# Optimization experiments

Measured on AMD Instinct MI355X. Metric: run time of the kernel, lower is better.

The kernel has to match this reference:

```python
import jax, jax.numpy as jnp
import numpy as np

N0, N1, N2, N3 = 600000, 100000, 20000, 4096
E0, E1, E2 = 1500000, 200000, 40960
D_IN, D_H, D_OUT = 100, 256, 47


def setup_inputs() -> dict:
    key = jax.random.key(0)
    ks = jax.random.split(key, 16)
    inp = {
        "x": jax.random.normal(ks[0], (N0, D_IN), jnp.float32),
        "ei0_src": jax.random.randint(ks[1], (E0,), 0, N0, jnp.int32),
        "ei0_dst": jax.random.randint(ks[2], (E0,), 0, N1, jnp.int32),
        "ei1_src": jax.random.randint(ks[3], (E1,), 0, N1, jnp.int32),
        "ei1_dst": jax.random.randint(ks[4], (E1,), 0, N2, jnp.int32),
        "ei2_src": jax.random.randint(ks[5], (E2,), 0, N2, jnp.int32),
        "ei2_dst": jax.random.randint(ks[6], (E2,), 0, N3, jnp.int32),
        "Wl0": jax.random.normal(ks[7], (D_IN, D_H), jnp.float32) * 0.1,
        "Wr0": jax.random.normal(ks[8], (D_IN, D_H), jnp.float32) * 0.1,
        "b0": jnp.zeros((D_H,), jnp.float32),
        "Wl1": jax.random.normal(ks[9], (D_H, D_H), jnp.float32) * 0.06,
        "Wr1": jax.random.normal(ks[10], (D_H, D_H), jnp.float32) * 0.06,
        "b1": jnp.zeros((D_H,), jnp.float32),
        "Wl2": jax.random.normal(ks[11], (D_H, D_OUT), jnp.float32) * 0.06,
        "Wr2": jax.random.normal(ks[12], (D_H, D_OUT), jnp.float32) * 0.06,
        "b2": jnp.zeros((D_OUT,), jnp.float32),
    }
    return inp


def _sage_layer(x_src, x_tgt, src, dst, n_tgt, Wl, Wr, b):
    # PyG SAGEConv (mean aggr): out = lin_l(mean_{j in N(i)} x_j) + lin_r(x_i)
    msgs = x_src[src]                                   # [E, d] gather
    s = jax.ops.segment_sum(msgs, dst, num_segments=n_tgt)
    cnt = jax.ops.segment_sum(jnp.ones((src.shape[0],), x_src.dtype), dst,
                              num_segments=n_tgt)[:, None]
    mean = s / jnp.maximum(cnt, 1.0)
    return mean @ Wl + x_tgt @ Wr + b


def reference(x, ei0_src, ei0_dst, ei1_src, ei1_dst, ei2_src, ei2_dst,
              Wl0, Wr0, b0, Wl1, Wr1, b1, Wl2, Wr2, b2):
    h = _sage_layer(x, x[:N1], ei0_src, ei0_dst, N1, Wl0, Wr0, b0)
    h = jax.nn.relu(h)  # dropout is identity in eval mode
    h = _sage_layer(h, h[:N2], ei1_src, ei1_dst, N2, Wl1, Wr1, b1)
    h = jax.nn.relu(h)
    h = _sage_layer(h, h[:N3], ei2_src, ei2_dst, N3, Wl2, Wr2, b2)
    return jax.nn.log_softmax(h, axis=-1)
```

## Files before the change

kernel.cpp:

```cpp
#include <hip/hip_runtime.h>

#define NN0 600000
#define NN1 100000
#define NN2 20000
#define NN3 4096
#define EE0 1500000
#define EE1 200000
#define EE2 40960
#define DIN 100
#define DH  256
#define DOUT 47
#define NTOT (NN1 + NN2 + NN3)

#define RNG 16384
#define CH0 32768
#define NC0 46
#define R0  7
#define CH1 16384
#define NC1 13
#define R1  2
#define CH2 8192
#define NC2 5
#define R2  1
#define HL0 (NC0 * R0)
#define HL1 (NC1 * R1)
#define HL2 (NC2 * R2)
#define HLT (HL0 + HL1 + HL2)
#define NGMAX 46
#define PACKB 27

#define NB0 98
#define NB1 20
#define NB2 4
#define NBT 122

#define HB0 5860
#define HB1 782
#define HB2 160
#define HBE (HB0 + HB1 + HB2)
#define CONVB 3072

typedef unsigned int uint;
typedef unsigned short ushort;
typedef __attribute__((ext_vector_type(8))) short bhalf8;
typedef __attribute__((ext_vector_type(4))) float f32x4;

union U16B {
    uint2  u2[2];
    uint4  u4;
    bhalf8 s8;
    ushort us[8];
};

__device__ __forceinline__ ushort f2bf(float f) {
    uint u = __float_as_uint(f);
    uint r = (u + 0x7FFFu + ((u >> 16) & 1u)) >> 16;
    return (ushort)r;
}
__device__ __forceinline__ float bf2f(uint bits16) {
    return __uint_as_float(bits16 << 16);
}

__device__ __forceinline__ void pack_one(const float* B, int K, int N, int NB,
                                         ushort* out, int bid, int l) {
    int kstep = bid / NB;
    int c = bid % NB;
    U16B v;
    #pragma unroll
    for (int j = 0; j < 8; ++j) {
        int k = kstep * 32 + ((l >> 4) << 3) + j;
        int col = (c << 4) | (l & 15);
        float f = (k < K && col < N) ? B[(size_t)k * N + col] : 0.0f;
        v.us[j] = f2bf(f);
    }
    *reinterpret_cast<bhalf8*>(out + ((size_t)bid * 64 + l) * 8) = v.s8;
}

__global__ __launch_bounds__(1024)
void hist_pack(const int* __restrict__ e0d, const int* __restrict__ e1d,
               const int* __restrict__ e2d, int* __restrict__ cntp,
               int* __restrict__ pos0, int* __restrict__ pos1,
               int* __restrict__ pos2,
               const float* __restrict__ Wl0, const float* __restrict__ Wr0,
               const float* __restrict__ Wl1, const float* __restrict__ Wr1,
               const float* __restrict__ Wl2, const float* __restrict__ Wr2,
               ushort* Bp0l, ushort* Bp0r, ushort* Bp1l, ushort* Bp1r,
               ushort* Bp2l, ushort* Bp2r) {
    __shared__ int lcnt[RNG];
    int b = blockIdx.x, tid = threadIdx.x;
    if (b >= HLT) {
        int bid = (b - HLT) * 16 + (tid >> 6);
        int l = tid & 63;
        if (bid < 64)       pack_one(Wl0, DIN, DH,  16, Bp0l, bid,       l);
        else if (bid < 128) pack_one(Wr0, DIN, DH,  16, Bp0r, bid - 64,  l);
        else if (bid < 256) pack_one(Wl1, DH,  DH,  16, Bp1l, bid - 128, l);
        else if (bid < 384) pack_one(Wr1, DH,  DH,  16, Bp1r, bid - 256, l);
        else if (bid < 408) pack_one(Wl2, DH,  DOUT, 3, Bp2l, bid - 384, l);
        else if (bid < 432) pack_one(Wr2, DH,  DOUT, 3, Bp2r, bid - 408, l);
        return;
    }
    const int* dstp; int E, CH, c, r, nbase, layerN;
    int* pos;
    if (b < HL0) {
        dstp = e0d; E = EE0; CH = CH0; c = b / R0; r = b % R0;
        nbase = 0; layerN = NN1; pos = pos0;
    } else if (b < HL0 + HL1) {
        int bb = b - HL0;
        dstp = e1d; E = EE1; CH = CH1; c = bb / R1; r = bb % R1;
        nbase = NN1; layerN = NN2; pos = pos1;
    } else {
        int bb = b - HL0 - HL1;
        dstp = e2d; E = EE2; CH = CH2; c = bb; r = 0;
        nbase = NN1 + NN2; layerN = NN3; pos = pos2;
    }
    for (int i = tid; i < RNG; i += 1024) lcnt[i] = 0;
    __syncthreads();
    int rbase = r * RNG;
    long long ebase = (long long)c * CH;
    for (int i = tid; i < CH; i += 1024) {
        int e = (int)(ebase + i);
        if (e < E) {
            int d = dstp[e];
            unsigned li = (unsigned)(d - rbase);
            if (li < RNG) pos[e] = atomicAdd(&lcnt[li], 1);
        }
    }
    __syncthreads();
    for (int i = tid; i < RNG; i += 1024) {
        int node = rbase + i;
        if (node < layerN)
            cntp[(size_t)c * NTOT + nbase + node] = lcnt[i];
    }
}

__device__ __forceinline__ void layer_of(int b, int& lb, int& n, int& po, int& cb) {
    if (b < NB0)      { lb = b;        n = NN1; po = 0;         cb = 0; }
    else if (b < NB0 + NB1) { lb = b - NB0;  n = NN2; po = NB0; cb = NN1; }
    else              { lb = b - NB0 - NB1; n = NN3; po = NB0 + NB1; cb = NN1 + NN2; }
}

__global__ __launch_bounds__(256)
void combScan1(int* __restrict__ cntp, int* __restrict__ cntAll,
               int* __restrict__ part) {
    int lb, n, po, cb;
    layer_of(blockIdx.x, lb, n, po, cb);
    int ng = (cb == 0) ? NC0 : (cb == NN1) ? NC1 : NC2;
    int base = lb * 1024;
    int sum = 0;
    #pragma unroll
    for (int jj = 0; jj < 4; ++jj) {
        int idx = base + threadIdx.x * 4 + jj;
        if (idx < n) {
            int i = cb + idx;
            int run = 0;
            for (int g = 0; g < ng; ++g) {
                size_t id = (size_t)g * NTOT + i;
                int v = cntp[id];
                cntp[id] = run;
                run += v;
            }
            cntAll[i] = run;
            sum += run;
        }
    }
    __shared__ int s[256];
    s[threadIdx.x] = sum;
    __syncthreads();
    for (int off = 128; off; off >>= 1) {
        if (threadIdx.x < off) s[threadIdx.x] += s[threadIdx.x + off];
        __syncthreads();
    }
    if (threadIdx.x == 0) part[po + lb] = s[0];
}

__global__ __launch_bounds__(256)
void scan3L(const int* __restrict__ cntAll, const int* __restrict__ part,
            int* __restrict__ rp0, int* __restrict__ rp1, int* __restrict__ rp2) {
    int lb, n, po, cb;
    layer_of(blockIdx.x, lb, n, po, cb);
    int* row_ptr;
    if (cb == 0)        row_ptr = rp0;
    else if (cb == NN1) row_ptr = rp1;
    else                row_ptr = rp2;

    __shared__ int partL[NBT];
    __shared__ int s[256];
    __shared__ int segOff;
    for (int i = threadIdx.x; i < NBT; i += 256) partL[i] = part[i];
    __syncthreads();
    if (threadIdx.x == 0) {
        int acc = 0;
        for (int k = 0; k < lb; ++k) acc += partL[po + k];
        segOff = acc;
    }
    __syncthreads();

    int base = lb * 1024;
    int v[4];
    int sum = 0;
    #pragma unroll
    for (int j = 0; j < 4; ++j) {
        int idx = base + threadIdx.x * 4 + j;
        v[j] = (idx < n) ? cntAll[cb + idx] : 0;
        sum += v[j];
    }
    s[threadIdx.x] = sum;
    __syncthreads();
    for (int off = 1; off < 256; off <<= 1) {
        int t = (threadIdx.x >= off) ? s[threadIdx.x - off] : 0;
        __syncthreads();
        s[threadIdx.x] += t;
        __syncthreads();
    }
    int off0 = segOff + s[threadIdx.x] - sum;
    #pragma unroll
    for (int j = 0; j < 4; ++j) {
        int idx = base + threadIdx.x * 4 + j;
        if (idx < n) {
            row_ptr[idx] = off0;
            off0 += v[j];
            if (idx == n - 1) row_ptr[n] = off0;
        }
    }
}

__global__ __launch_bounds__(256)
void place_conv(const int* __restrict__ e0s, const int* __restrict__ e0d,
                const int* __restrict__ e1s, const int* __restrict__ e1d,
                const int* __restrict__ e2s, const int* __restrict__ e2d,
                const int* __restrict__ pos0, const int* __restrict__ pos1,
                const int* __restrict__ pos2, const int* __restrict__ cntp,
                const int* __restrict__ rp0, const int* __restrict__ rp1,
                const int* __restrict__ rp2,
                int* __restrict__ eidx0, int* __restrict__ eidx1,
                int* __restrict__ eidx2,
                const float* __restrict__ x, ushort* __restrict__ xb,
                long long n4) {
    int b = blockIdx.x;
    int tid = threadIdx.x;
    if (b < HB0) {
        int e = b * 256 + tid;
        if (e < EE0) {
            int d = e0d[e];
            int g = e >> 15;
            int p = rp0[d] + cntp[(size_t)g * NTOT + d] + pos0[e];
            eidx0[p] = e0s[e];
        }
    } else if (b < HB0 + HB1) {
        int e = (b - HB0) * 256 + tid;
        if (e < EE1) {
            int d = e1d[e];
            int g = e >> 14;
            int p = rp1[d] + cntp[(size_t)g * NTOT + NN1 + d] + pos1[e];
            eidx1[p] = e1s[e];
        }
    } else if (b < HBE) {
        int e = (b - HB0 - HB1) * 256 + tid;
        if (e < EE2) {
            int d = e2d[e];
            int g = e >> 13;
            int p = rp2[d] + cntp[(size_t)g * NTOT + NN1 + NN2 + d] + pos2[e];
            eidx2[p] = e2s[e];
        }
    } else {
        long long cb = b - HBE;
        for (long long t = cb * 256 + tid; t < n4; t += (long long)CONVB * 256) {
            float4 v = *reinterpret_cast<const float4*>(x + t * 4);
            uint2 o;
            o.x = (uint)f2bf(v.x) | ((uint)f2bf(v.y) << 16);
            o.y = (uint)f2bf(v.z) | ((uint)f2bf(v.w) << 16);
            *reinterpret_cast<uint2*>(xb + t * 4) = o;
        }
    }
}


__global__ __launch_bounds__(256)
void agg100_b(const ushort* __restrict__ xb, const int* __restrict__ rp,
              const int* __restrict__ eidx, ushort* __restrict__ out, int nNodes) {
    int node = blockIdx.x * 8 + (threadIdx.x >> 5);
    if (node >= nNodes) return;
    int hl = threadIdx.x & 31;
    bool act = hl < 25;
    int beg = rp[node], end = rp[node + 1];
    float a0 = 0.f, a1 = 0.f, a2 = 0.f, a3 = 0.f;
    int j = beg;
    for (; j + 7 < end; j += 8) {
        int sidx[8];
        #pragma unroll
        for (int q = 0; q < 8; ++q) sidx[q] = eidx[j + q];
        if (act) {
            uint2 vv[8];
            #pragma unroll
            for (int q = 0; q < 8; ++q)
                vv[q] = *reinterpret_cast<const uint2*>(xb + (size_t)sidx[q] * DIN + hl * 4);
            #pragma unroll
            for (int q = 0; q < 8; ++q) {
                a0 += bf2f(vv[q].x & 0xffffu);
                a1 += bf2f(vv[q].x >> 16);
                a2 += bf2f(vv[q].y & 0xffffu);
                a3 += bf2f(vv[q].y >> 16);
            }
        }
    }
    for (; j < end; ++j) {
        int s0 = eidx[j];
        if (act) {
            uint2 v0 = *reinterpret_cast<const uint2*>(xb + (size_t)s0 * DIN + hl * 4);
            a0 += bf2f(v0.x & 0xffffu);
            a1 += bf2f(v0.x >> 16);
            a2 += bf2f(v0.y & 0xffffu);
            a3 += bf2f(v0.y >> 16);
        }
    }
    float inv = 1.0f / fmaxf((float)(end - beg), 1.0f);
    if (act) {
        uint2 o;
        o.x = (uint)f2bf(a0 * inv) | ((uint)f2bf(a1 * inv) << 16);
        o.y = (uint)f2bf(a2 * inv) | ((uint)f2bf(a3 * inv) << 16);
        *reinterpret_cast<uint2*>(out + (size_t)node * DIN + hl * 4) = o;
    }
}

__global__ __launch_bounds__(256)
void agg256_b(const ushort* __restrict__ h, const int* __restrict__ rp,
              const int* __restrict__ eidx, ushort* __restrict__ out, int nNodes) {
    int node = blockIdx.x * 4 + (threadIdx.x >> 6);
    if (node >= nNodes) return;
    int l = threadIdx.x & 63;
    int beg = rp[node], end = rp[node + 1];
    float a0 = 0.f, a1 = 0.f, a2 = 0.f, a3 = 0.f;
    int j = beg;
    for (; j + 7 < end; j += 8) {
        int sidx[8];
        #pragma unroll
        for (int q = 0; q < 8; ++q) sidx[q] = eidx[j + q];
        uint2 vv[8];
        #pragma unroll
        for (int q = 0; q < 8; ++q)
            vv[q] = *reinterpret_cast<const uint2*>(h + (size_t)sidx[q] * DH + l * 4);
        #pragma unroll
        for (int q = 0; q < 8; ++q) {
            a0 += bf2f(vv[q].x & 0xffffu);
            a1 += bf2f(vv[q].x >> 16);
            a2 += bf2f(vv[q].y & 0xffffu);
            a3 += bf2f(vv[q].y >> 16);
        }
    }
    for (; j < end; ++j) {
        int s0 = eidx[j];
        uint2 v0 = *reinterpret_cast<const uint2*>(h + (size_t)s0 * DH + l * 4);
        a0 += bf2f(v0.x & 0xffffu);
        a1 += bf2f(v0.x >> 16);
        a2 += bf2f(v0.y & 0xffffu);
        a3 += bf2f(v0.y >> 16);
    }
    float inv = 1.0f / fmaxf((float)(end - beg), 1.0f);
    uint2 o;
    o.x = (uint)f2bf(a0 * inv) | ((uint)f2bf(a1 * inv) << 16);
    o.y = (uint)f2bf(a2 * inv) | ((uint)f2bf(a3 * inv) << 16);
    *reinterpret_cast<uint2*>(out + (size_t)node * DH + l * 4) = o;
}

template <int RELU, int OUTBF>
__global__ __launch_bounds__(256)
void gemm_dual(const ushort* __restrict__ A1, int K1, int S1, int str1,
               const ushort* __restrict__ A2, int K2, int S2, int str2,
               const ushort* __restrict__ B1p, const ushort* __restrict__ B2p,
               const float* __restrict__ bias, void* __restrict__ Cv,
               int M, int N, int NB, int NBW, int Cstride) {
    __shared__ ushort At[2][2048];

    const int tid = threadIdx.x;
    const int w = tid >> 6;
    const int l = tid & 63;
    const int m0 = blockIdx.x * 64;
    const int S = S1 + S2;

    f32x4 acc[4][4];
    #pragma unroll
    for (int m = 0; m < 4; ++m)
        #pragma unroll
        for (int i = 0; i < 4; ++i)
            acc[m][i] = f32x4{0.f, 0.f, 0.f, 0.f};

    auto stage = [&](int s, int buf) {
        const ushort* A; int str, Keff, ks;
        if (s < S1) { A = A1; str = str1; Keff = K1; ks = s; }
        else        { A = A2; str = str2; Keff = K2; ks = s - S1; }
        int r  = tid >> 2;
        int kc = tid & 3;
        int row = m0 + r;
        int k = ks * 32 + (kc << 3);
        U16B v;
        v.u4.x = v.u4.y = v.u4.z = v.u4.w = 0u;
        if (row < M && k < Keff) {
            const ushort* p = A + (size_t)row * str + k;
            v.u2[0] = *reinterpret_cast<const uint2*>(p);
            v.u2[1] = *reinterpret_cast<const uint2*>(p + 4);
            if (k + 8 > Keff) {
                #pragma unroll
                for (int j = 0; j < 8; ++j)
                    if (k + j >= Keff) v.us[j] = 0;
            }
        }
        int slot = ((r >> 4) << 6) | (r & 15) | (kc << 4);
        *reinterpret_cast<bhalf8*>(&At[buf][slot * 8]) = v.s8;
    };

    stage(0, 0);
    __syncthreads();

    for (int s = 0; s < S; ++s) {
        int buf = s & 1;
        if (s + 1 < S) stage(s + 1, buf ^ 1);

        const ushort* Bp; int ks;
        if (s < S1) { Bp = B1p; ks = s; }
        else        { Bp = B2p; ks = s - S1; }

        bhalf8 a[4];
        #pragma unroll
        for (int m = 0; m < 4; ++m)
            a[m] = *reinterpret_cast<bhalf8*>(&At[buf][((m << 6) | l) * 8]);

        #pragma unroll
        for (int i = 0; i < 4; ++i) {
            if (i < NBW) {
                int c = w * NBW + i;
                if (c < NB) {
                    bhalf8 b = *reinterpret_cast<const bhalf8*>(
                        Bp + ((size_t)(ks * NB + c) * 64 + l) * 8);
                    #pragma unroll
                    for (int m = 0; m < 4; ++m)
                        acc[m][i] = __builtin_amdgcn_mfma_f32_16x16x32_bf16(
                            a[m], b, acc[m][i], 0, 0, 0);
                }
            }
        }
        __syncthreads();
    }

    #pragma unroll
    for (int i = 0; i < 4; ++i) {
        if (i >= NBW) continue;
        int c = w * NBW + i;
        if (c >= NB) continue;
        int col = (c << 4) | (l & 15);
        if (col >= N) continue;
        float bb = bias[col];
        #pragma unroll
        for (int m = 0; m < 4; ++m) {
            #pragma unroll
            for (int e = 0; e < 4; ++e) {
                int row = m0 + (m << 4) + ((l >> 4) << 2) + e;
                if (row < M) {
                    float v = acc[m][i][e] + bb;
                    if (RELU) v = fmaxf(v, 0.0f);
                    if (OUTBF)
                        ((ushort*)Cv)[(size_t)row * Cstride + col] = f2bf(v);
                    else
                        ((float*)Cv)[(size_t)row * Cstride + col] = v;
                }
            }
        }
    }
}

__global__ void log_softmax_47(const float* __restrict__ z, float* __restrict__ out) {
    int row = blockIdx.x;
    int lane = threadIdx.x;
    float v = (lane < DOUT) ? z[(size_t)row * DOUT + lane] : -INFINITY;
    float m = v;
    #pragma unroll
    for (int off = 32; off; off >>= 1) m = fmaxf(m, __shfl_xor(m, off));
    float e = (lane < DOUT) ? expf(v - m) : 0.0f;
    float s = e;
    #pragma unroll
    for (int off = 32; off; off >>= 1) s += __shfl_xor(s, off);
    if (lane < DOUT) out[(size_t)row * DOUT + lane] = v - m - logf(s);
}

extern "C" void kernel_launch(void* const* d_in, const int* in_sizes, int n_in,
                              void* d_out, int out_size, void* d_ws, size_t ws_size,
                              hipStream_t stream) {
    const float* x   = (const float*)d_in[0];
    const int* e0s   = (const int*)d_in[1];
    const int* e0d   = (const int*)d_in[2];
    const int* e1s   = (const int*)d_in[3];
    const int* e1d   = (const int*)d_in[4];
    const int* e2s   = (const int*)d_in[5];
    const int* e2d   = (const int*)d_in[6];
    const float* Wl0 = (const float*)d_in[7];
    const float* Wr0 = (const float*)d_in[8];
    const float* b0  = (const float*)d_in[9];
    const float* Wl1 = (const float*)d_in[10];
    const float* Wr1 = (const float*)d_in[11];
    const float* b1  = (const float*)d_in[12];
    const float* Wl2 = (const float*)d_in[13];
    const float* Wr2 = (const float*)d_in[14];
    const float* b2  = (const float*)d_in[15];

    char* ws = (char*)d_ws;
    size_t off = 0;
    auto alloc = [&](size_t bytes) -> void* {
        void* p = ws + off;
        off += (bytes + 255) & ~(size_t)255;
        return p;
    };

    ushort* agg0b = (ushort*)alloc((size_t)NN1 * DIN * 2);
    ushort* h1    = (ushort*)alloc((size_t)NN1 * DH * 2);
    ushort* agg1b = (ushort*)alloc((size_t)NN2 * DH * 2);
    ushort* h2    = (ushort*)alloc((size_t)NN2 * DH * 2);
    ushort* agg2b = (ushort*)alloc((size_t)NN3 * DH * 2);
    float*  z     = (float*)alloc((size_t)NN3 * DOUT * 4);

    ushort* Bp0l = (ushort*)alloc((size_t)4 * 16 * 64 * 8 * 2);
    ushort* Bp0r = (ushort*)alloc((size_t)4 * 16 * 64 * 8 * 2);
    ushort* Bp1l = (ushort*)alloc((size_t)8 * 16 * 64 * 8 * 2);
    ushort* Bp1r = (ushort*)alloc((size_t)8 * 16 * 64 * 8 * 2);
    ushort* Bp2l = (ushort*)alloc((size_t)8 * 3 * 64 * 8 * 2);
    ushort* Bp2r = (ushort*)alloc((size_t)8 * 3 * 64 * 8 * 2);

    int* cntp   = (int*)alloc((size_t)NGMAX * NTOT * 4);
    int* cntAll = (int*)alloc((size_t)NTOT * 4);
    int* pos0   = (int*)alloc((size_t)EE0 * 4);
    int* pos1   = (int*)alloc((size_t)EE1 * 4);
    int* pos2   = (int*)alloc((size_t)EE2 * 4);
    int* rp0    = (int*)alloc((size_t)(NN1 + 1) * 4);
    int* eidx0  = (int*)alloc((size_t)EE0 * 4);
    int* rp1    = (int*)alloc((size_t)(NN2 + 1) * 4);
    int* eidx1  = (int*)alloc((size_t)EE1 * 4);
    int* rp2    = (int*)alloc((size_t)(NN3 + 1) * 4);
    int* eidx2  = (int*)alloc((size_t)EE2 * 4);
    int* part   = (int*)alloc(256 * 4);
    ushort* xb  = (ushort*)alloc((size_t)NN0 * DIN * 2 + 256);

    hist_pack<<<HLT + PACKB, 1024, 0, stream>>>(
        e0d, e1d, e2d, cntp, pos0, pos1, pos2,
        Wl0, Wr0, Wl1, Wr1, Wl2, Wr2,
        Bp0l, Bp0r, Bp1l, Bp1r, Bp2l, Bp2r);

    combScan1<<<NBT, 256, 0, stream>>>(cntp, cntAll, part);
    scan3L<<<NBT, 256, 0, stream>>>(cntAll, part, rp0, rp1, rp2);

    {
        long long n4 = (long long)NN0 * DIN / 4;
        place_conv<<<HBE + CONVB, 256, 0, stream>>>(
            e0s, e0d, e1s, e1d, e2s, e2d, pos0, pos1, pos2, cntp,
            rp0, rp1, rp2, eidx0, eidx1, eidx2, x, xb, n4);
    }

    agg100_b<<<(NN1 + 7) / 8, 256, 0, stream>>>(xb, rp0, eidx0, agg0b, NN1);
    gemm_dual<1, 1><<<(NN1 + 63) / 64, 256, 0, stream>>>(
        agg0b, DIN, 4, DIN, xb, DIN, 4, DIN, Bp0l, Bp0r, b0, h1,
        NN1, DH, 16, 4, DH);

    agg256_b<<<(NN2 + 3) / 4, 256, 0, stream>>>(h1, rp1, eidx1, agg1b, NN2);
    gemm_dual<1, 1><<<(NN2 + 63) / 64, 256, 0, stream>>>(
        agg1b, DH, 8, DH, h1, DH, 8, DH, Bp1l, Bp1r, b1, h2,
        NN2, DH, 16, 4, DH);

    agg256_b<<<(NN3 + 3) / 4, 256, 0, stream>>>(h2, rp2, eidx2, agg2b, NN3);
    gemm_dual<0, 0><<<(NN3 + 63) / 64, 256, 0, stream>>>(
        agg2b, DH, 8, DH, h2, DH, 8, DH, Bp2l, Bp2r, b2, z,
        NN3, DOUT, 3, 1, DOUT);

    log_softmax_47<<<NN3, 64, 0, stream>>>(z, (float*)d_out);
}
```

Baseline: 456.7 us.

## Drop separate fp32-to-bf16 conversion pass and read fp32 input directly

```diff
diff --git a/kernel.cpp b/kernel.cpp
--- a/kernel.cpp
+++ b/kernel.cpp
@@ -38,7 +38,6 @@
 #define HB1 782
 #define HB2 160
 #define HBE (HB0 + HB1 + HB2)
-#define CONVB 3072
 
 typedef unsigned int uint;
 typedef unsigned short ushort;
@@ -225,17 +224,15 @@
 }
 
 __global__ __launch_bounds__(256)
-void place_conv(const int* __restrict__ e0s, const int* __restrict__ e0d,
-                const int* __restrict__ e1s, const int* __restrict__ e1d,
-                const int* __restrict__ e2s, const int* __restrict__ e2d,
-                const int* __restrict__ pos0, const int* __restrict__ pos1,
-                const int* __restrict__ pos2, const int* __restrict__ cntp,
-                const int* __restrict__ rp0, const int* __restrict__ rp1,
-                const int* __restrict__ rp2,
-                int* __restrict__ eidx0, int* __restrict__ eidx1,
-                int* __restrict__ eidx2,
-                const float* __restrict__ x, ushort* __restrict__ xb,
-                long long n4) {
+void place_all(const int* __restrict__ e0s, const int* __restrict__ e0d,
+               const int* __restrict__ e1s, const int* __restrict__ e1d,
+               const int* __restrict__ e2s, const int* __restrict__ e2d,
+               const int* __restrict__ pos0, const int* __restrict__ pos1,
+               const int* __restrict__ pos2, const int* __restrict__ cntp,
+               const int* __restrict__ rp0, const int* __restrict__ rp1,
+               const int* __restrict__ rp2,
+               int* __restrict__ eidx0, int* __restrict__ eidx1,
+               int* __restrict__ eidx2) {
     int b = blockIdx.x;
     int tid = threadIdx.x;
     if (b < HB0) {
@@ -254,7 +251,7 @@
             int p = rp1[d] + cntp[(size_t)g * NTOT + NN1 + d] + pos1[e];
             eidx1[p] = e1s[e];
         }
-    } else if (b < HBE) {
+    } else {
         int e = (b - HB0 - HB1) * 256 + tid;
         if (e < EE2) {
             int d = e2d[e];
@@ -262,21 +259,12 @@
             int p = rp2[d] + cntp[(size_t)g * NTOT + NN1 + NN2 + d] + pos2[e];
             eidx2[p] = e2s[e];
         }
-    } else {
-        long long cb = b - HBE;
-        for (long long t = cb * 256 + tid; t < n4; t += (long long)CONVB * 256) {
-            float4 v = *reinterpret_cast<const float4*>(x + t * 4);
-            uint2 o;
-            o.x = (uint)f2bf(v.x) | ((uint)f2bf(v.y) << 16);
-            o.y = (uint)f2bf(v.z) | ((uint)f2bf(v.w) << 16);
-            *reinterpret_cast<uint2*>(xb + t * 4) = o;
-        }
     }
 }
 
 
 __global__ __launch_bounds__(256)
-void agg100_b(const ushort* __restrict__ xb, const int* __restrict__ rp,
+void agg100_f(const float* __restrict__ x, const int* __restrict__ rp,
               const int* __restrict__ eidx, ushort* __restrict__ out, int nNodes) {
     int node = blockIdx.x * 8 + (threadIdx.x >> 5);
     if (node >= nNodes) return;
@@ -290,27 +278,21 @@
         #pragma unroll
         for (int q = 0; q < 8; ++q) sidx[q] = eidx[j + q];
         if (act) {
-            uint2 vv[8];
+            float4 vv[8];
             #pragma unroll
             for (int q = 0; q < 8; ++q)
-                vv[q] = *reinterpret_cast<const uint2*>(xb + (size_t)sidx[q] * DIN + hl * 4);
+                vv[q] = *reinterpret_cast<const float4*>(x + (size_t)sidx[q] * DIN + hl * 4);
             #pragma unroll
             for (int q = 0; q < 8; ++q) {
-                a0 += bf2f(vv[q].x & 0xffffu);
-                a1 += bf2f(vv[q].x >> 16);
-                a2 += bf2f(vv[q].y & 0xffffu);
-                a3 += bf2f(vv[q].y >> 16);
+                a0 += vv[q].x; a1 += vv[q].y; a2 += vv[q].z; a3 += vv[q].w;
             }
         }
     }
     for (; j < end; ++j) {
         int s0 = eidx[j];
         if (act) {
-            uint2 v0 = *reinterpret_cast<const uint2*>(xb + (size_t)s0 * DIN + hl * 4);
-            a0 += bf2f(v0.x & 0xffffu);
-            a1 += bf2f(v0.x >> 16);
-            a2 += bf2f(v0.y & 0xffffu);
-            a3 += bf2f(v0.y >> 16);
+            float4 v0 = *reinterpret_cast<const float4*>(x + (size_t)s0 * DIN + hl * 4);
+            a0 += v0.x; a1 += v0.y; a2 += v0.z; a3 += v0.w;
         }
     }
     float inv = 1.0f / fmaxf((float)(end - beg), 1.0f);
@@ -362,10 +344,10 @@
     *reinterpret_cast<uint2*>(out + (size_t)node * DH + l * 4) = o;
 }
 
-template <int RELU, int OUTBF>
+template <int RELU, int OUTBF, int A2F32>
 __global__ __launch_bounds__(256)
 void gemm_dual(const ushort* __restrict__ A1, int K1, int S1, int str1,
-               const ushort* __restrict__ A2, int K2, int S2, int str2,
+               const void* __restrict__ A2, int K2, int S2, int str2,
                const ushort* __restrict__ B1p, const ushort* __restrict__ B2p,
                const float* __restrict__ bias, void* __restrict__ Cv,
                int M, int N, int NB, int NBW, int Cstride) {
@@ -385,23 +367,45 @@
             acc[m][i] = f32x4{0.f, 0.f, 0.f, 0.f};
 
     auto stage = [&](int s, int buf) {
-        const ushort* A; int str, Keff, ks;
-        if (s < S1) { A = A1; str = str1; Keff = K1; ks = s; }
-        else        { A = A2; str = str2; Keff = K2; ks = s - S1; }
         int r  = tid >> 2;
         int kc = tid & 3;
         int row = m0 + r;
-        int k = ks * 32 + (kc << 3);
         U16B v;
         v.u4.x = v.u4.y = v.u4.z = v.u4.w = 0u;
-        if (row < M && k < Keff) {
-            const ushort* p = A + (size_t)row * str + k;
-            v.u2[0] = *reinterpret_cast<const uint2*>(p);
-            v.u2[1] = *reinterpret_cast<const uint2*>(p + 4);
-            if (k + 8 > Keff) {
-                #pragma unroll
-                for (int j = 0; j < 8; ++j)
-                    if (k + j >= Keff) v.us[j] = 0;
+        if (s < S1) {
+            int k = s * 32 + (kc << 3);
+            if (row < M && k < K1) {
+                const ushort* p = A1 + (size_t)row * str1 + k;
+                v.u2[0] = *reinterpret_cast<const uint2*>(p);
+                v.u2[1] = *reinterpret_cast<const uint2*>(p + 4);
+                if (k + 8 > K1) {
+                    #pragma unroll
+                    for (int j = 0; j < 8; ++j)
+                        if (k + j >= K1) v.us[j] = 0;
+                }
+            }
+        } else {
+            int ks = s - S1;
+            int k = ks * 32 + (kc << 3);
+            if (row < M && k < K2) {
+                if (A2F32) {
+                    const float* p = (const float*)A2 + (size_t)row * str2 + k;
+                    float4 f0 = *reinterpret_cast<const float4*>(p);
+                    float4 f1 = *reinterpret_cast<const float4*>(p + 4);
+                    v.us[0] = f2bf(f0.x); v.us[1] = f2bf(f0.y);
+                    v.us[2] = f2bf(f0.z); v.us[3] = f2bf(f0.w);
+                    v.us[4] = f2bf(f1.x); v.us[5] = f2bf(f1.y);
+                    v.us[6] = f2bf(f1.z); v.us[7] = f2bf(f1.w);
+                } else {
+                    const ushort* p = (const ushort*)A2 + (size_t)row * str2 + k;
+                    v.u2[0] = *reinterpret_cast<const uint2*>(p);
+                    v.u2[1] = *reinterpret_cast<const uint2*>(p + 4);
+                }
+                if (k + 8 > K2) {
+                    #pragma unroll
+                    for (int j = 0; j < 8; ++j)
+                        if (k + j >= K2) v.us[j] = 0;
+                }
             }
         }
         int slot = ((r >> 4) << 6) | (r & 15) | (kc << 4);
@@ -535,7 +539,6 @@
     int* rp2    = (int*)alloc((size_t)(NN3 + 1) * 4);
     int* eidx2  = (int*)alloc((size_t)EE2 * 4);
     int* part   = (int*)alloc(256 * 4);
-    ushort* xb  = (ushort*)alloc((size_t)NN0 * DIN * 2 + 256);
 
     hist_pack<<<HLT + PACKB, 1024, 0, stream>>>(
         e0d, e1d, e2d, cntp, pos0, pos1, pos2,
@@ -545,26 +548,23 @@
     combScan1<<<NBT, 256, 0, stream>>>(cntp, cntAll, part);
     scan3L<<<NBT, 256, 0, stream>>>(cntAll, part, rp0, rp1, rp2);
 
-    {
-        long long n4 = (long long)NN0 * DIN / 4;
-        place_conv<<<HBE + CONVB, 256, 0, stream>>>(
-            e0s, e0d, e1s, e1d, e2s, e2d, pos0, pos1, pos2, cntp,
-            rp0, rp1, rp2, eidx0, eidx1, eidx2, x, xb, n4);
-    }
-
-    agg100_b<<<(NN1 + 7) / 8, 256, 0, stream>>>(xb, rp0, eidx0, agg0b, NN1);
-    gemm_dual<1, 1><<<(NN1 + 63) / 64, 256, 0, stream>>>(
-        agg0b, DIN, 4, DIN, xb, DIN, 4, DIN, Bp0l, Bp0r, b0, h1,
+    place_all<<<HBE, 256, 0, stream>>>(e0s, e0d, e1s, e1d, e2s, e2d,
+                                       pos0, pos1, pos2, cntp,
+                                       rp0, rp1, rp2, eidx0, eidx1, eidx2);
+
+    agg100_f<<<(NN1 + 7) / 8, 256, 0, stream>>>(x, rp0, eidx0, agg0b, NN1);
+    gemm_dual<1, 1, 1><<<(NN1 + 63) / 64, 256, 0, stream>>>(
+        agg0b, DIN, 4, DIN, (const void*)x, DIN, 4, DIN, Bp0l, Bp0r, b0, h1,
         NN1, DH, 16, 4, DH);
 
     agg256_b<<<(NN2 + 3) / 4, 256, 0, stream>>>(h1, rp1, eidx1, agg1b, NN2);
-    gemm_dual<1, 1><<<(NN2 + 63) / 64, 256, 0, stream>>>(
-        agg1b, DH, 8, DH, h1, DH, 8, DH, Bp1l, Bp1r, b1, h2,
+    gemm_dual<1, 1, 0><<<(NN2 + 63) / 64, 256, 0, stream>>>(
+        agg1b, DH, 8, DH, (const void*)h1, DH, 8, DH, Bp1l, Bp1r, b1, h2,
         NN2, DH, 16, 4, DH);
 
     agg256_b<<<(NN3 + 3) / 4, 256, 0, stream>>>(h2, rp2, eidx2, agg2b, NN3);
-    gemm_dual<0, 0><<<(NN3 + 63) / 64, 256, 0, stream>>>(
-        agg2b, DH, 8, DH, h2, DH, 8, DH, Bp2l, Bp2r, b2, z,
+    gemm_dual<0, 0, 0><<<(NN3 + 63) / 64, 256, 0, stream>>>(
+        agg2b, DH, 8, DH, (const void*)h2, DH, 8, DH, Bp2l, Bp2r, b2, z,
         NN3, DOUT, 3, 1, DOUT);
 
     log_softmax_47<<<NN3, 64, 0, stream>>>(z, (float*)d_out);
```

Result: faster. 426.5 us (-6.6%).
